# Kernel optimization log

Measured on AMD Instinct MI355X. Metric: run time of the kernel, lower is better.

## Reference

```python
import jax, jax.numpy as jnp
import numpy as np
import math

HIDDEN = 1024
NUM_HEADS = 16
NUM_GROUPS = 16  # source einsum/rearrange only shape-checks when groups == heads
HEAD_DIM = HIDDEN // NUM_HEADS


def rope(x, base=10000.0):
    # x: [b, s, d]; applied to the FULL hidden vector before head split, as in source.
    # Source rope_fn has a reshape bug; this is the intended rotate-half RoPE with
    # half_d frequencies 1/base^(i/half_d) (== 1/base^(2i/d)).
    b, s, d = x.shape
    half = d // 2
    x1, x2 = x[..., :half], x[..., half:]
    pos = jnp.arange(s, dtype=x.dtype)[:, None]                          # [s,1]
    inv_freq = 1.0 / (base ** (jnp.arange(half, dtype=x.dtype) / half))  # [half]
    ang = pos * inv_freq[None, :]                                        # [s,half]
    sin = jnp.sin(ang)[None]                                             # [1,s,half]
    cos = jnp.cos(ang)[None]
    return jnp.concatenate([x1 * cos - x2 * sin, x2 * cos + x1 * sin], axis=-1)


def setup_inputs() -> dict:
    key = jax.random.key(0)
    ks = jax.random.split(key, 10)
    scale = 1.0 / math.sqrt(HIDDEN)
    inp = {
        "x": jax.random.normal(ks[0], (2, 2048, HIDDEN), dtype=jnp.float32),
        "attn_mask": jax.random.randint(ks[1], (2, 2048), 0, 2, dtype=jnp.int32),
        "Wq": jax.random.uniform(ks[2], (HIDDEN, HIDDEN), jnp.float32, -scale, scale),
        "bq": jax.random.uniform(ks[3], (HIDDEN,), jnp.float32, -scale, scale),
        "Wk": jax.random.uniform(ks[4], (HIDDEN, HIDDEN), jnp.float32, -scale, scale),
        "bk": jax.random.uniform(ks[5], (HIDDEN,), jnp.float32, -scale, scale),
        "Wv": jax.random.uniform(ks[6], (HIDDEN, HIDDEN), jnp.float32, -scale, scale),
        "bv": jax.random.uniform(ks[7], (HIDDEN,), jnp.float32, -scale, scale),
        "Wo": jax.random.uniform(ks[8], (HIDDEN, HIDDEN), jnp.float32, -scale, scale),
        "bo": jax.random.uniform(ks[9], (HIDDEN,), jnp.float32, -scale, scale),
    }
    return inp


def reference(x, attn_mask, Wq, bq, Wk, bk, Wv, bv, Wo, bo):
    b, s, _ = x.shape
    g = NUM_GROUPS
    subh = NUM_HEADS // g  # = 1 here
    d = HIDDEN // g        # per-group dim (== head dim when g == h)

    q = rope(x @ Wq.T + bq)
    k = rope(x @ Wk.T + bk)
    v = x @ Wv.T + bv

    # q: b s (g subh d) -> b g subh s d ; k,v: b s (g d) -> b g s d
    q = q.reshape(b, s, g, subh, d).transpose(0, 2, 3, 1, 4)
    k = k.reshape(b, s, g, d).transpose(0, 2, 1, 3)
    v = v.reshape(b, s, g, d).transpose(0, 2, 1, 3)

    e = jnp.einsum('bghqd,bgkd->bghqk', q, k) / math.sqrt(HEAD_DIM)  # [b,g,subh,s,s]
    mask5 = attn_mask[:, None, None, None, :]  # broadcast over g, subh, query
    e = jnp.where(mask5 == 0, -jnp.inf, e)
    attn = jax.nn.softmax(e, axis=-1)
    out = jnp.einsum('bghqk,bgkd->bghqd', attn, v)            # [b,g,subh,s,d]
    out = out.transpose(0, 3, 1, 2, 4).reshape(b, s, HIDDEN)  # b s (g subh d)
    return out @ Wo.T + bo
```

## Files before the change

kernel.cpp:

```cpp
#include <hip/hip_runtime.h>
#include <hip/hip_bf16.h>


constexpr int Bb  = 2;
constexpr int Ss  = 2048;
constexpr int Hh  = 1024;
constexpr int NHh = 16;
constexpr int Mm  = Bb * Ss;

typedef __attribute__((ext_vector_type(8))) unsigned short ushort8;
typedef __attribute__((ext_vector_type(8))) short short8;
typedef __attribute__((ext_vector_type(4))) float f32x4;
typedef __attribute__((ext_vector_type(4))) unsigned int u32x4;

__device__ __forceinline__ unsigned short f2bf(float f) {
    unsigned int u = __float_as_uint(f);
    u += 0x7fffu + ((u >> 16) & 1u);
    return (unsigned short)(u >> 16);
}
__device__ __forceinline__ float bf2f(unsigned short h) {
    return __uint_as_float(((unsigned int)h) << 16);
}
__device__ __forceinline__ void gload16(const void* g, void* l) {
    __builtin_amdgcn_global_load_lds(
        (const __attribute__((address_space(1))) unsigned int*)g,
        (__attribute__((address_space(3))) unsigned int*)l, 16, 0, 0);
}

__global__ __launch_bounds__(256) void convert_k(
    const float* __restrict__ x,
    const float* __restrict__ Wq, const float* __restrict__ Wk,
    const float* __restrict__ Wv, const float* __restrict__ Wo,
    unsigned short* __restrict__ xb, unsigned short* __restrict__ wall)
{
    size_t e = ((size_t)blockIdx.x * 256 + threadIdx.x) << 3;
    const float* s; unsigned short* d;
    if (e < (size_t)Mm * Hh) {
        s = x + e; d = xb + e;
    } else {
        size_t f = e - (size_t)Mm * Hh;
        int t = (int)(f >> 20);
        const float* w = (t == 0) ? Wq : (t == 1) ? Wk : (t == 2) ? Wv : Wo;
        s = w + (f & 1048575);
        d = wall + f;
    }
    float4 a = *(const float4*)s;
    float4 b = *(const float4*)(s + 4);
    ushort8 o;
    o[0] = f2bf(a.x); o[1] = f2bf(a.y); o[2] = f2bf(a.z); o[3] = f2bf(a.w);
    o[4] = f2bf(b.x); o[5] = f2bf(b.y); o[6] = f2bf(b.z); o[7] = f2bf(b.w);
    *(ushort8*)d = o;
}

#define GEMM_BODY(ATYPE_PTR, WPTR, K0MAX)                                          \
    __shared__ unsigned short As[128 * 64];                                        \
    __shared__ unsigned short Bs[128 * 64];                                        \
    const int tid  = threadIdx.x;                                                  \
    const int lane = tid & 63;                                                     \
    const int w    = tid >> 6;                                                     \
    const int wr   = w >> 1, wc = w & 1;                                           \
    const int l16  = lane & 15, g = lane >> 4;                                     \
    const int R0   = blockIdx.x * 128;                                             \
    char* asb = (char*)As; char* bsb = (char*)Bs;                                  \
    f32x4 acc[4][4] = {};                                                          \
    for (int k0 = 0; k0 < K0MAX; k0 += 64) {                                       \
        _Pragma("unroll")                                                          \
        for (int it = 0; it < 4; ++it) {                                           \
            int sbase = w * 4096 + it * 1024;                                      \
            int boff  = sbase + lane * 16;                                         \
            int r     = boff >> 7;                                                 \
            int c     = (boff >> 4) & 7;                                           \
            int col   = k0 + ((c ^ (r & 7)) << 3);                                 \
            gload16(&ATYPE_PTR[(size_t)(R0 + r) * 1024 + col], asb + sbase);       \
            gload16(&WPTR[(size_t)(gn + r) * 1024 + col], bsb + sbase);            \
        }                                                                          \
        __syncthreads();                                                           \
        short8 bfrag[4][2];                                                        \
        _Pragma("unroll")                                                          \
        for (int u = 0; u < 4; ++u) {                                              \
            int row = wc * 64 + u * 16 + l16;                                      \
            _Pragma("unroll")                                                      \
            for (int s = 0; s < 2; ++s)                                            \
                bfrag[u][s] = *(const short8*)(bsb + row * 128 +                   \
                               ((s * 64 + g * 16) ^ ((row & 7) << 4)));            \
        }                                                                          \
        _Pragma("unroll")                                                          \
        for (int t = 0; t < 4; ++t) {                                              \
            int row = wr * 64 + t * 16 + l16;                                      \
            short8 af[2];                                                          \
            _Pragma("unroll")                                                      \
            for (int s = 0; s < 2; ++s)                                            \
                af[s] = *(const short8*)(asb + row * 128 +                         \
                         ((s * 64 + g * 16) ^ ((row & 7) << 4)));                  \
            _Pragma("unroll")                                                      \
            for (int u = 0; u < 4; ++u) {                                          \
                acc[t][u] = __builtin_amdgcn_mfma_f32_16x16x32_bf16(af[0], bfrag[u][0], acc[t][u], 0, 0, 0); \
                acc[t][u] = __builtin_amdgcn_mfma_f32_16x16x32_bf16(af[1], bfrag[u][1], acc[t][u], 0, 0, 0); \
            }                                                                      \
        }                                                                          \
        __syncthreads();                                                           \
    }

__global__ __launch_bounds__(256) void gemm_qkv_k(
    const unsigned short* __restrict__ xb, const unsigned short* __restrict__ wall,
    const float* __restrict__ bq, const float* __restrict__ bk, const float* __restrict__ bv,
    unsigned short* __restrict__ q, unsigned short* __restrict__ k2,
    unsigned short* __restrict__ v)
{
    const int gn = blockIdx.y * 128;
    GEMM_BODY(xb, wall, 1024)

    const int sel = gn >> 10;
    const int n0  = gn & 1023;
    const float* bias = (sel == 0) ? bq : (sel == 1) ? bk : bv;
    unsigned short* outp = (sel == 0) ? q : (sel == 1) ? k2 : v;
    const float qs = (sel == 0) ? 0.18033688011112042f : 1.0f;
    #pragma unroll
    for (int u = 0; u < 4; ++u) {
        int coll = wc * 64 + u * 16 + l16;
        float bb = bias[n0 + coll];
        #pragma unroll
        for (int t = 0; t < 4; ++t)
            #pragma unroll
            for (int rr = 0; rr < 4; ++rr) {
                int row = R0 + wr * 64 + t * 16 + g * 4 + rr;
                outp[(size_t)row * 1024 + n0 + coll] = f2bf((acc[t][u][rr] + bb) * qs);
            }
    }
}

__global__ __launch_bounds__(256) void gemm_out_k(
    const unsigned short* __restrict__ ao, const unsigned short* __restrict__ wo,
    const float* __restrict__ bo, float* __restrict__ out)
{
    const int gn = blockIdx.y * 128;
    GEMM_BODY(ao, wo, 1024)

    #pragma unroll
    for (int u = 0; u < 4; ++u) {
        int coll = wc * 64 + u * 16 + l16;
        float bb = bo[gn + coll];
        #pragma unroll
        for (int t = 0; t < 4; ++t)
            #pragma unroll
            for (int rr = 0; rr < 4; ++rr) {
                int row = R0 + wr * 64 + t * 16 + g * 4 + rr;
                out[(size_t)row * 1024 + gn + coll] = acc[t][u][rr] + bb;
            }
    }
}

__global__ __launch_bounds__(256) void rope_frag_k(
    const unsigned short* __restrict__ qin, const unsigned short* __restrict__ kin,
    unsigned short* __restrict__ qfrag, unsigned short* __restrict__ kfrag)
{
    __shared__ unsigned short Ld[2][64][72];
    const int kt = blockIdx.x;
    const int hp = blockIdx.y;
    const int zz = blockIdx.z;
    const int bz = zz & 1, sel = zz >> 1;
    const unsigned short* src = sel ? kin : qin;
    unsigned short* dstf = sel ? kfrag : qfrag;

    const int t   = threadIdx.x;
    const int r   = t & 63;
    const int c16 = (t >> 6) << 4;
    const int pos = kt * 64 + r;
    const size_t rowb = (size_t)(bz * Ss + pos) * 1024;

    ushort8 A0 = *(const ushort8*)&src[rowb + hp * 64 + c16];
    ushort8 A1 = *(const ushort8*)&src[rowb + hp * 64 + c16 + 8];
    ushort8 B0 = *(const ushort8*)&src[rowb + (hp + 8) * 64 + c16];
    ushort8 B1 = *(const ushort8*)&src[rowb + (hp + 8) * 64 + c16 + 8];

    #pragma unroll
    for (int i = 0; i < 16; ++i) {
        int d = c16 + i;
        float jj  = (float)(hp * 64 + d);
        float inv = exp2f(jj * -0.0259525632621414f);
        float ang = (float)pos * inv;
        float sn, cs;
        __sincosf(ang, &sn, &cs);
        unsigned short ua = (i < 8) ? A0[i] : A1[i - 8];
        unsigned short ub = (i < 8) ? B0[i] : B1[i - 8];
        float a = bf2f(ua), b = bf2f(ub);
        Ld[0][r][d] = f2bf(a * cs - b * sn);
        Ld[1][r][d] = f2bf(b * cs + a * sn);
    }
    __syncthreads();

    #pragma unroll
    for (int cc = 0; cc < 4; ++cc) {
        int c    = t * 4 + cc;
        int hh   = c >> 9;
        int ci   = c & 511;
        int blk  = ci >> 7, s2 = (ci >> 6) & 1, lane2 = ci & 63;
        int gg = lane2 >> 4, ll = lane2 & 15;
        ushort8 o = *(const ushort8*)&Ld[hh][blk * 16 + ll][s2 * 32 + gg * 8];
        size_t base = (size_t)(bz * 16 + hp + hh * 8) * 131072 + (size_t)kt * 4096;
        *(ushort8*)&dstf[base + (size_t)ci * 8] = o;
    }
}

__global__ __launch_bounds__(256) void fragify_v_k(
    const unsigned short* __restrict__ v, unsigned short* __restrict__ vfrag)
{
    __shared__ unsigned short Ld[64][72];
    const int kt = blockIdx.x, bh = blockIdx.y;
    const int bz = bh >> 4, h = bh & 15;
    const int t = threadIdx.x;
    const int r = t & 63, c0 = (t >> 6) << 4;
    const unsigned short* srcp = &v[(size_t)(bz * Ss + kt * 64 + r) * 1024 + h * 64 + c0];
    *(ushort8*)&Ld[r][c0]     = *(const ushort8*)srcp;
    *(ushort8*)&Ld[r][c0 + 8] = *(const ushort8*)(srcp + 8);
    __syncthreads();

    #pragma unroll
    for (int cc = 0; cc < 2; ++cc) {
        int c = t * 2 + cc;
        int dt4 = c >> 7, ks = (c >> 6) & 1, lane2 = c & 63;
        int gg = lane2 >> 4, ll = lane2 & 15;
        ushort8 o;
        #pragma unroll
        for (int e = 0; e < 8; ++e)
            o[e] = Ld[ks * 32 + gg * 8 + e][dt4 * 16 + ll];
        *(ushort8*)&vfrag[(size_t)bh * 131072 + (size_t)kt * 4096 + (size_t)c * 8] = o;
    }
}

#define FLASH_ITER(KC, KN, KT)                                                     \
    {                                                                              \
        const int ktn = kt0 + ((((KT) - kt0) + 1) & 15);                           \
        _Pragma("unroll")                                                          \
        for (int i = 0; i < 8; ++i)                                                \
            KN[i] = *(const short8*)&kfb[(size_t)ktn * 4096 + i * 512 + lane * 8]; \
        _Pragma("unroll")                                                          \
        for (int i = 0; i < 8; ++i)                                                \
            VV[i] = *(const short8*)&vfb[(size_t)(KT) * 4096 + i * 512 + lane * 8];\
        int mk[4][4];                                                              \
        _Pragma("unroll")                                                          \
        for (int k4 = 0; k4 < 4; ++k4)                                             \
            *(int4*)&mk[k4][0] =                                                   \
                *(const int4*)&mask[bz * Ss + (KT) * 64 + k4 * 16 + g * 4];        \
        f32x4 S[2][4];                                                             \
        _Pragma("unroll")                                                          \
        for (int t = 0; t < 2; ++t)                                                \
            _Pragma("unroll")                                                      \
            for (int k4 = 0; k4 < 4; ++k4) S[t][k4] = (f32x4)0.f;                  \
        _Pragma("unroll")                                                          \
        for (int k4 = 0; k4 < 4; ++k4)                                             \
            _Pragma("unroll")                                                      \
            for (int t = 0; t < 2; ++t) {                                          \
                S[t][k4] = __builtin_amdgcn_mfma_f32_16x16x32_bf16(                \
                    KC[k4 * 2 + 0], qf[t][0], S[t][k4], 0, 0, 0);                  \
                S[t][k4] = __builtin_amdgcn_mfma_f32_16x16x32_bf16(                \
                    KC[k4 * 2 + 1], qf[t][1], S[t][k4], 0, 0, 0);                  \
            }                                                                      \
        _Pragma("unroll")                                                          \
        for (int t = 0; t < 2; ++t)                                                \
            _Pragma("unroll")                                                      \
            for (int k4 = 0; k4 < 4; ++k4)                                         \
                _Pragma("unroll")                                                  \
                for (int r = 0; r < 4; ++r)                                        \
                    S[t][k4][r] = mk[k4][r] ? S[t][k4][r] : -1e30f;                \
        float rm[2];                                                               \
        _Pragma("unroll")                                                          \
        for (int t = 0; t < 2; ++t) {                                              \
            float m0 = fmaxf(fmaxf(S[t][0][0], S[t][0][1]), fmaxf(S[t][0][2], S[t][0][3])); \
            float m1 = fmaxf(fmaxf(S[t][1][0], S[t][1][1]), fmaxf(S[t][1][2], S[t][1][3])); \
            float m2 = fmaxf(fmaxf(S[t][2][0], S[t][2][1]), fmaxf(S[t][2][2], S[t][2][3])); \
            float m3 = fmaxf(fmaxf(S[t][3][0], S[t][3][1]), fmaxf(S[t][3][2], S[t][3][3])); \
            float m  = fmaxf(fmaxf(m0, m1), fmaxf(m2, m3));                        \
            m = fmaxf(m, __shfl_xor(m, 16));                                       \
            m = fmaxf(m, __shfl_xor(m, 32));                                       \
            rm[t] = m;                                                             \
        }                                                                          \
        bool grow = (rm[0] > mrow[0] + 10.0f) || (rm[1] > mrow[1] + 10.0f);        \
        if (__any((int)grow)) {                                                    \
            float mn0 = fmaxf(mrow[0], rm[0]);                                     \
            float mn1 = fmaxf(mrow[1], rm[1]);                                     \
            float rs0 = exp2f(mrow[0] - mn0);                                      \
            float rs1 = exp2f(mrow[1] - mn1);                                      \
            mrow[0] = mn0; mrow[1] = mn1;                                          \
            _Pragma("unroll")                                                      \
            for (int r = 0; r < 4; ++r) {                                          \
                float f0 = __shfl(rs0, g * 4 + r);                                 \
                float f1 = __shfl(rs1, g * 4 + r);                                 \
                _Pragma("unroll")                                                  \
                for (int dt = 0; dt < 4; ++dt) { O[0][dt][r] *= f0; O[1][dt][r] *= f1; } \
                Osum[0][r] *= f0; Osum[1][r] *= f1;                                \
            }                                                                      \
        }                                                                          \
        _Pragma("unroll")                                                          \
        for (int t = 0; t < 2; ++t) {                                              \
            unsigned int U[4][2];                                                  \
            _Pragma("unroll")                                                      \
            for (int k4 = 0; k4 < 4; ++k4) {                                       \
                float p0 = exp2f(S[t][k4][0] - mrow[t]);                           \
                float p1 = exp2f(S[t][k4][1] - mrow[t]);                           \
                float p2 = exp2f(S[t][k4][2] - mrow[t]);                           \
                float p3 = exp2f(S[t][k4][3] - mrow[t]);                           \
                asm("v_cvt_pk_bf16_f32 %0, %1, %2" : "=v"(U[k4][0]) : "v"(p0), "v"(p1)); \
                asm("v_cvt_pk_bf16_f32 %0, %1, %2" : "=v"(U[k4][1]) : "v"(p2), "v"(p3)); \
            }                                                                      \
            asm("v_permlane32_swap_b32 %0, %1" : "+v"(U[0][0]), "+v"(U[1][0]));    \
            asm("v_permlane32_swap_b32 %0, %1" : "+v"(U[0][1]), "+v"(U[1][1]));    \
            asm("v_permlane32_swap_b32 %0, %1" : "+v"(U[2][0]), "+v"(U[3][0]));    \
            asm("v_permlane32_swap_b32 %0, %1" : "+v"(U[2][1]), "+v"(U[3][1]));    \
            asm("v_permlane16_swap_b32 %0, %1" : "+v"(U[0][0]), "+v"(U[1][0]));    \
            asm("v_permlane16_swap_b32 %0, %1" : "+v"(U[0][1]), "+v"(U[1][1]));    \
            asm("v_permlane16_swap_b32 %0, %1" : "+v"(U[2][0]), "+v"(U[3][0]));    \
            asm("v_permlane16_swap_b32 %0, %1" : "+v"(U[2][1]), "+v"(U[3][1]));    \
            _Pragma("unroll")                                                      \
            for (int ks = 0; ks < 2; ++ks) {                                       \
                u32x4 gp;                                                          \
                gp[0] = U[2 * ks][0]; gp[1] = U[2 * ks][1];                        \
                gp[2] = U[2 * ks + 1][0]; gp[3] = U[2 * ks + 1][1];                \
                short8 pf = __builtin_bit_cast(short8, gp);                        \
                Osum[t] = __builtin_amdgcn_mfma_f32_16x16x32_bf16(pf, ones, Osum[t], 0, 0, 0); \
                _Pragma("unroll")                                                  \
                for (int dt = 0; dt < 4; ++dt)                                     \
                    O[t][dt] = __builtin_amdgcn_mfma_f32_16x16x32_bf16(            \
                        pf, VV[dt * 2 + ks], O[t][dt], 0, 0, 0);                   \
            }                                                                      \
        }                                                                          \
    }

__global__ __launch_bounds__(256) void flash_k(
    const unsigned short* __restrict__ qfrag, const unsigned short* __restrict__ kfrag,
    const unsigned short* __restrict__ vfrag, const int* __restrict__ mask,
    unsigned short* __restrict__ opart, float2* __restrict__ ml)
{
    const int F   = blockIdx.x;
    const int xcd = F & 7, j = F >> 3;
    const int grp = xcd * 4 + (j >> 5);
    const int rem = j & 31;
    const int qb  = rem >> 1;
    const int half = rem & 1;
    const int h   = grp & 15;
    const int bz  = grp >> 4;
    const int kt0 = half * 16;

    const int tid  = threadIdx.x;
    const int lane = tid & 63;
    const int w    = tid >> 6;
    const int l16  = lane & 15;
    const int g    = lane >> 4;

    const size_t fb = (size_t)(bz * 16 + h) * 131072;
    const unsigned short* kfb = kfrag + fb;
    const unsigned short* vfb = vfrag + fb;
    const unsigned short* qfb = qfrag + fb;

    short8 qf[2][2];
    #pragma unroll
    for (int t = 0; t < 2; ++t)
        #pragma unroll
        for (int s = 0; s < 2; ++s)
            qf[t][s] = *(const short8*)&qfb[(size_t)(qb * 8 + w * 2 + t) * 1024
                                            + s * 512 + lane * 8];

    f32x4 O[2][4];
    #pragma unroll
    for (int t = 0; t < 2; ++t)
        #pragma unroll
        for (int d = 0; d < 4; ++d) O[t][d] = (f32x4)0.f;
    f32x4 Osum[2];
    Osum[0] = (f32x4)0.f; Osum[1] = (f32x4)0.f;
    float mrow[2] = {-1.0e4f, -1.0e4f};

    short8 ones;
    #pragma unroll
    for (int e = 0; e < 8; ++e) ones[e] = (short)0x3F80;

    short8 KA[8], KB[8], VV[8];
    #pragma unroll
    for (int i = 0; i < 8; ++i)
        KA[i] = *(const short8*)&kfb[(size_t)kt0 * 4096 + i * 512 + lane * 8];

    for (int kt2 = 0; kt2 < 16; kt2 += 2) {
        FLASH_ITER(KA, KB, kt0 + kt2)
        FLASH_ITER(KB, KA, kt0 + kt2 + 1)
    }

    const size_t NE = (size_t)Mm * Hh;
    #pragma unroll
    for (int t = 0; t < 2; ++t)
        #pragma unroll
        for (int r = 0; r < 4; ++r) {
            float osum = Osum[t][r];
            float inv  = osum > 0.f ? 1.0f / osum : 0.f;
            float mo   = __shfl(mrow[t], g * 4 + r);
            int rowl   = qb * 128 + w * 32 + t * 16 + g * 4 + r;
            size_t ob  = (size_t)half * NE
                       + ((size_t)(bz * Ss + rowl)) * 1024 + h * 64;
            #pragma unroll
            for (int dt = 0; dt < 4; ++dt)
                opart[ob + dt * 16 + l16] = f2bf(O[t][dt][r] * inv);
            if (l16 == 0)
                ml[((half * 2 + bz) * 16 + h) * 2048 + rowl] = make_float2(mo, osum);
        }
}

__global__ __launch_bounds__(256) void combine_k(
    const unsigned short* __restrict__ opart, const float2* __restrict__ ml,
    unsigned short* __restrict__ ao)
{
    const size_t NE = (size_t)Mm * Hh;
    int c    = blockIdx.x * 256 + threadIdx.x;
    int row  = c >> 7;
    int col8 = c & 127;
    int h    = col8 >> 3;
    int bz   = row >> 11, qrow = row & 2047;

    float2 a = ml[((0 * 2 + bz) * 16 + h) * 2048 + qrow];
    float2 b = ml[((1 * 2 + bz) * 16 + h) * 2048 + qrow];
    float M  = fmaxf(a.x, b.x);
    float w1 = exp2f(a.x - M) * a.y;
    float w2 = exp2f(b.x - M) * b.y;
    float tot = w1 + w2;
    float inv = tot > 0.f ? 1.0f / tot : 0.f;
    w1 *= inv; w2 *= inv;

    ushort8 o1 = *(const ushort8*)&opart[(size_t)c * 8];
    ushort8 o2 = *(const ushort8*)&opart[NE + (size_t)c * 8];
    ushort8 o;
    #pragma unroll
    for (int jj = 0; jj < 8; ++jj)
        o[jj] = f2bf(bf2f(o1[jj]) * w1 + bf2f(o2[jj]) * w2);
    *(ushort8*)&ao[(size_t)c * 8] = o;
}

extern "C" void kernel_launch(void* const* d_in, const int* in_sizes, int n_in,
                              void* d_out, int out_size, void* d_ws, size_t ws_size,
                              hipStream_t stream)
{
    const float* x  = (const float*)d_in[0];
    const int*   am = (const int*)d_in[1];
    const float* Wq = (const float*)d_in[2];
    const float* bq = (const float*)d_in[3];
    const float* Wk = (const float*)d_in[4];
    const float* bk = (const float*)d_in[5];
    const float* Wv = (const float*)d_in[6];
    const float* bv = (const float*)d_in[7];
    const float* Wo = (const float*)d_in[8];
    const float* bo = (const float*)d_in[9];
    float* out = (float*)d_out;

    const size_t NE = (size_t)Mm * Hh;
    unsigned short* q     = (unsigned short*)d_ws;
    unsigned short* k     = q + NE;
    unsigned short* v     = k + NE;
    unsigned short* ao    = v + NE;
    unsigned short* xb    = ao + NE;
    unsigned short* wall  = xb + NE;
    unsigned short* wo    = wall + 3u * 1048576u;
    unsigned short* kfrag = wall + 4u * 1048576u;
    unsigned short* qfrag = xb;
    unsigned short* vfrag = q;
    unsigned short* opart = k;
    float2*         ml    = (float2*)(kfrag + 4u * 1048576u);

    convert_k<<<(2 * NE) / (256 * 8), 256, 0, stream>>>(x, Wq, Wk, Wv, Wo, xb, wall);
    gemm_qkv_k<<<dim3(Mm / 128, 3072 / 128), 256, 0, stream>>>(
        xb, wall, bq, bk, bv, q, k, v);
    rope_frag_k<<<dim3(32, 8, 4), 256, 0, stream>>>(q, k, qfrag, kfrag);
    fragify_v_k<<<dim3(32, 32), 256, 0, stream>>>(v, vfrag);
    flash_k<<<dim3(1024), 256, 0, stream>>>(qfrag, kfrag, vfrag, am, opart, ml);
    combine_k<<<dim3((Mm * 128) / 256), 256, 0, stream>>>(opart, ml, ao);
    gemm_out_k<<<dim3(Mm / 128, Hh / 128), 256, 0, stream>>>(ao, wo, bo, out);
}
```

Measured before the change: 187.1 us.

## Fold key mask into V fragments and row-sum MFMA instead of masking scores

Removes the per-element masking of the score tile in the flash loop. Masked keys now have their V rows zeroed during V fragmentation, and the softmax denominator is accumulated with an MFMA against a bf16 0/1 mask vector instead of a ones vector, so masked keys add nothing to either sum. A small kernel converts the int mask to bf16, and the flash kernel gains a launch_bounds occupancy hint. The risk is that the running max now includes masked scores, which is still mathematically valid but can change rescaling behaviour.

```diff
diff --git a/kernel.cpp b/kernel.cpp
--- a/kernel.cpp
+++ b/kernel.cpp
@@ -50,6 +50,13 @@
     o[0] = f2bf(a.x); o[1] = f2bf(a.y); o[2] = f2bf(a.z); o[3] = f2bf(a.w);
     o[4] = f2bf(b.x); o[5] = f2bf(b.y); o[6] = f2bf(b.z); o[7] = f2bf(b.w);
     *(ushort8*)d = o;
+}
+
+__global__ __launch_bounds__(256) void maskbf_k(
+    const int* __restrict__ am, unsigned short* __restrict__ maskbf)
+{
+    int i = blockIdx.x * 256 + threadIdx.x;
+    maskbf[i] = am[i] ? (unsigned short)0x3F80 : (unsigned short)0;
 }
 
 #define GEMM_BODY(ATYPE_PTR, WPTR, K0MAX)                                          \
@@ -203,9 +210,11 @@
 }
 
 __global__ __launch_bounds__(256) void fragify_v_k(
-    const unsigned short* __restrict__ v, unsigned short* __restrict__ vfrag)
+    const unsigned short* __restrict__ v, const int* __restrict__ mask,
+    unsigned short* __restrict__ vfrag)
 {
     __shared__ unsigned short Ld[64][72];
+    __shared__ int Lm[64];
     const int kt = blockIdx.x, bh = blockIdx.y;
     const int bz = bh >> 4, h = bh & 15;
     const int t = threadIdx.x;
@@ -213,6 +222,7 @@
     const unsigned short* srcp = &v[(size_t)(bz * Ss + kt * 64 + r) * 1024 + h * 64 + c0];
     *(ushort8*)&Ld[r][c0]     = *(const ushort8*)srcp;
     *(ushort8*)&Ld[r][c0 + 8] = *(const ushort8*)(srcp + 8);
+    if (t < 64) Lm[t] = mask[bz * Ss + kt * 64 + t];
     __syncthreads();
 
     #pragma unroll
@@ -222,8 +232,10 @@
         int gg = lane2 >> 4, ll = lane2 & 15;
         ushort8 o;
         #pragma unroll
-        for (int e = 0; e < 8; ++e)
-            o[e] = Ld[ks * 32 + gg * 8 + e][dt4 * 16 + ll];
+        for (int e = 0; e < 8; ++e) {
+            int key = ks * 32 + gg * 8 + e;
+            o[e] = Lm[key] ? Ld[key][dt4 * 16 + ll] : (unsigned short)0;
+        }
         *(ushort8*)&vfrag[(size_t)bh * 131072 + (size_t)kt * 4096 + (size_t)c * 8] = o;
     }
 }
@@ -237,11 +249,9 @@
         _Pragma("unroll")                                                          \
         for (int i = 0; i < 8; ++i)                                                \
             VV[i] = *(const short8*)&vfb[(size_t)(KT) * 4096 + i * 512 + lane * 8];\
-        int mk[4][4];                                                              \
-        _Pragma("unroll")                                                          \
-        for (int k4 = 0; k4 < 4; ++k4)                                             \
-            *(int4*)&mk[k4][0] =                                                   \
-                *(const int4*)&mask[bz * Ss + (KT) * 64 + k4 * 16 + g * 4];        \
+        short8 mf[2];                                                              \
+        mf[0] = *(const short8*)&mbz[(KT) * 64 + g * 8];                           \
+        mf[1] = *(const short8*)&mbz[(KT) * 64 + 32 + g * 8];                      \
         f32x4 S[2][4];                                                             \
         _Pragma("unroll")                                                          \
         for (int t = 0; t < 2; ++t)                                                \
@@ -256,13 +266,6 @@
                 S[t][k4] = __builtin_amdgcn_mfma_f32_16x16x32_bf16(                \
                     KC[k4 * 2 + 1], qf[t][1], S[t][k4], 0, 0, 0);                  \
             }                                                                      \
-        _Pragma("unroll")                                                          \
-        for (int t = 0; t < 2; ++t)                                                \
-            _Pragma("unroll")                                                      \
-            for (int k4 = 0; k4 < 4; ++k4)                                         \
-                _Pragma("unroll")                                                  \
-                for (int r = 0; r < 4; ++r)                                        \
-                    S[t][k4][r] = mk[k4][r] ? S[t][k4][r] : -1e30f;                \
         float rm[2];                                                               \
         _Pragma("unroll")                                                          \
         for (int t = 0; t < 2; ++t) {                                              \
@@ -317,7 +320,7 @@
                 gp[0] = U[2 * ks][0]; gp[1] = U[2 * ks][1];                        \
                 gp[2] = U[2 * ks + 1][0]; gp[3] = U[2 * ks + 1][1];                \
                 short8 pf = __builtin_bit_cast(short8, gp);                        \
-                Osum[t] = __builtin_amdgcn_mfma_f32_16x16x32_bf16(pf, ones, Osum[t], 0, 0, 0); \
+                Osum[t] = __builtin_amdgcn_mfma_f32_16x16x32_bf16(pf, mf[ks], Osum[t], 0, 0, 0); \
                 _Pragma("unroll")                                                  \
                 for (int dt = 0; dt < 4; ++dt)                                     \
                     O[t][dt] = __builtin_amdgcn_mfma_f32_16x16x32_bf16(            \
@@ -326,9 +329,9 @@
         }                                                                          \
     }
 
-__global__ __launch_bounds__(256) void flash_k(
+__global__ __launch_bounds__(256, 2) void flash_k(
     const unsigned short* __restrict__ qfrag, const unsigned short* __restrict__ kfrag,
-    const unsigned short* __restrict__ vfrag, const int* __restrict__ mask,
+    const unsigned short* __restrict__ vfrag, const unsigned short* __restrict__ maskbf,
     unsigned short* __restrict__ opart, float2* __restrict__ ml)
 {
     const int F   = blockIdx.x;
@@ -351,6 +354,7 @@
     const unsigned short* kfb = kfrag + fb;
     const unsigned short* vfb = vfrag + fb;
     const unsigned short* qfb = qfrag + fb;
+    const unsigned short* mbz = maskbf + bz * Ss;
 
     short8 qf[2][2];
     #pragma unroll
@@ -368,10 +372,6 @@
     f32x4 Osum[2];
     Osum[0] = (f32x4)0.f; Osum[1] = (f32x4)0.f;
     float mrow[2] = {-1.0e4f, -1.0e4f};
-
-    short8 ones;
-    #pragma unroll
-    for (int e = 0; e < 8; ++e) ones[e] = (short)0x3F80;
 
     short8 KA[8], KB[8], VV[8];
     #pragma unroll
@@ -460,13 +460,15 @@
     unsigned short* vfrag = q;
     unsigned short* opart = k;
     float2*         ml    = (float2*)(kfrag + 4u * 1048576u);
+    unsigned short* maskbf = (unsigned short*)(ml + 131072);
 
     convert_k<<<(2 * NE) / (256 * 8), 256, 0, stream>>>(x, Wq, Wk, Wv, Wo, xb, wall);
+    maskbf_k<<<dim3(Mm / 256), 256, 0, stream>>>(am, maskbf);
     gemm_qkv_k<<<dim3(Mm / 128, 3072 / 128), 256, 0, stream>>>(
         xb, wall, bq, bk, bv, q, k, v);
     rope_frag_k<<<dim3(32, 8, 4), 256, 0, stream>>>(q, k, qfrag, kfrag);
-    fragify_v_k<<<dim3(32, 32), 256, 0, stream>>>(v, vfrag);
-    flash_k<<<dim3(1024), 256, 0, stream>>>(qfrag, kfrag, vfrag, am, opart, ml);
+    fragify_v_k<<<dim3(32, 32), 256, 0, stream>>>(v, am, vfrag);
+    flash_k<<<dim3(1024), 256, 0, stream>>>(qfrag, kfrag, vfrag, maskbf, opart, ml);
     combine_k<<<dim3((Mm * 128) / 256), 256, 0, stream>>>(opart, ml, ao);
     gemm_out_k<<<dim3(Mm / 128, Hh / 128), 256, 0, stream>>>(ao, wo, bo, out);
 }
```

Result: faster. 162.1 us (-13.4%).
